# Optimization experiments

Measured on AMD Instinct MI355X. Metric: run time of the kernel, lower is better.

The kernel has to match this reference:

```python
import jax, jax.numpy as jnp
import numpy as np

D_MODEL = 256
B, H, T = 4, 8, 2048
EPS = 1e-8


def _clinear(x_r, x_i, w_r, w_i, b_r, b_i):
    # complex matmul: (x_r + i x_i) @ (w_r + i w_i)^T + (b_r + i b_i)
    y_r = jnp.matmul(x_r, w_r.T) - jnp.matmul(x_i, w_i.T) + b_r
    y_i = jnp.matmul(x_i, w_r.T) + jnp.matmul(x_r, w_i.T) + b_i
    return y_r, y_i


def setup_inputs() -> dict:
    key = jax.random.key(0)
    ks = jax.random.split(key, 24)
    d = D_MODEL
    std = np.sqrt(2.0 / (d + d)) / np.sqrt(2.0)  # glorot-ish * 1/sqrt(2) as in _init_weights
    inp = {}
    inp['q_in_r'] = jax.random.normal(ks[0], (B, H, T, d), jnp.float32)
    inp['q_in_i'] = jax.random.normal(ks[1], (B, H, T, d), jnp.float32)
    inp['kv_in_r'] = jax.random.normal(ks[2], (B, H, T, d), jnp.float32)
    inp['kv_in_i'] = jax.random.normal(ks[3], (B, H, T, d), jnp.float32)
    i = 4
    for p in ['q', 'k', 'v', 'o']:
        inp[p + '_wr'] = std * jax.random.normal(ks[i], (d, d), jnp.float32); i += 1
        inp[p + '_wi'] = std * jax.random.normal(ks[i], (d, d), jnp.float32); i += 1
        inp[p + '_br'] = jnp.zeros((d,), jnp.float32)
        inp[p + '_bi'] = jnp.zeros((d,), jnp.float32)
    inp['gate_w'] = std * jax.random.normal(ks[i], (d, d), jnp.float32)
    inp['gate_b'] = jnp.zeros((d,), jnp.float32)
    return inp


def reference(q_in_r, q_in_i, kv_in_r, kv_in_i,
              q_wr, q_wi, q_br, q_bi,
              k_wr, k_wi, k_br, k_bi,
              v_wr, v_wi, v_br, v_bi,
              o_wr, o_wi, o_br, o_bi,
              gate_w, gate_b):
    D = q_in_r.shape[-1]
    q_r, q_i = _clinear(q_in_r, q_in_i, q_wr, q_wi, q_br, q_bi)
    k_r, k_i = _clinear(kv_in_r, kv_in_i, k_wr, k_wi, k_br, k_bi)
    v_r, v_i = _clinear(kv_in_r, kv_in_i, v_wr, v_wi, v_br, v_bi)
    scale = 1.0 / np.sqrt(D)
    # real part of complex inner product <q, k> (the module's dual-part score)
    scores = (jnp.einsum('bhqd,bhkd->bhqk', q_r, k_r)
              + jnp.einsum('bhqd,bhkd->bhqk', q_i, k_i)) * scale
    attn = jax.nn.softmax(scores, axis=-1)
    ctx_r = jnp.einsum('bhqk,bhkd->bhqd', attn, v_r)
    ctx_i = jnp.einsum('bhqk,bhkd->bhqd', attn, v_i)
    out_r, out_i = _clinear(ctx_r, ctx_i, o_wr, o_wi, o_br, o_bi)
    out_mag = jnp.sqrt(out_r ** 2 + out_i ** 2 + EPS)
    gate = jax.nn.sigmoid(jnp.matmul(out_mag, gate_w.T) + gate_b)
    return out_r * gate, out_i * gate
```

## Files before the change

### kernel.cpp

```cpp
#include <hip/hip_runtime.h>
#include <hip/hip_bf16.h>
#include <hip/hip_fp16.h>
#include <stdint.h>


#define TSEQ   2048
#define NHEADS 32
#define MTOT   65536
#define DDC    512
#define HCHUNK 8

typedef float    f32x4  __attribute__((ext_vector_type(4)));
typedef _Float16 f16x8  __attribute__((ext_vector_type(8)));
typedef uint16_t u16x4  __attribute__((ext_vector_type(4)));
typedef uint16_t u16x8  __attribute__((ext_vector_type(8)));

__device__ __forceinline__ uint16_t f2h(float f) {
  _Float16 h = (_Float16)f;
  return __builtin_bit_cast(uint16_t, h);
}
__device__ __forceinline__ float h2f(uint16_t u) {
  return (float)__builtin_bit_cast(_Float16, u);
}

__device__ __forceinline__ void gld16(const void* g, void* l) {
  __builtin_amdgcn_global_load_lds(
      (const __attribute__((address_space(1))) uint32_t*)g,
      (__attribute__((address_space(3))) uint32_t*)l, 16, 0, 0);
}

enum { EP_F16Z = 0, EP_PROJ = 1, EP_OUT = 2, EP_GATE = 3 };

template <int EP>
__global__ __launch_bounds__(256, 2) void gemm_bt(
    const uint16_t* __restrict__ A, int lda, long zA,
    const uint16_t* __restrict__ B, int ldb, long zB,
    void* __restrict__ C, int ldc, long zC, int K,
    const float* __restrict__ biasR, const float* __restrict__ biasI,
    float scale, float* __restrict__ outR, float* __restrict__ outI) {
  __shared__ uint16_t lA[128 * 32];
  __shared__ uint16_t lB[128 * 32];
  const int tid  = threadIdx.x;
  const int wave = tid >> 6;
  const int lane = tid & 63;
  const int wr   = (wave >> 1) * 64;
  const int wc   = (wave & 1) * 64;
  const long tm  = (long)blockIdx.y * 128;
  const long tn  = (long)blockIdx.x * 128;
  const uint16_t* Ab = A + (long)blockIdx.z * zA;
  const uint16_t* Bb = B + (long)blockIdx.z * zB;

  f32x4 acc[4][4] = {};

  const int  srow  = wave * 16 + (lane >> 2);
  const int  skoff = (lane & 3) * 8;
  uint16_t* lA0 = &lA[(wave * 16) * 32];
  uint16_t* lA1 = &lA[(64 + wave * 16) * 32];
  uint16_t* lB0 = &lB[(wave * 16) * 32];
  uint16_t* lB1 = &lB[(64 + wave * 16) * 32];

  const int fr = lane & 15;
  const int fk = (lane >> 4) * 8;

  const int nK = K >> 5;
  for (int kb = 0; kb < nK; ++kb) {
    const long k0 = (long)kb * 32 + skoff;
    __syncthreads();
    gld16(Ab + (tm + srow) * (long)lda + k0,      lA0);
    gld16(Ab + (tm + 64 + srow) * (long)lda + k0, lA1);
    gld16(Bb + (tn + srow) * (long)ldb + k0,      lB0);
    gld16(Bb + (tn + 64 + srow) * (long)ldb + k0, lB1);
    __syncthreads();

    f16x8 af[4], bf[4];
#pragma unroll
    for (int i = 0; i < 4; ++i)
      af[i] = *(const f16x8*)&lA[(wr + i * 16 + fr) * 32 + fk];
#pragma unroll
    for (int j = 0; j < 4; ++j)
      bf[j] = *(const f16x8*)&lB[(wc + j * 16 + fr) * 32 + fk];
#pragma unroll
    for (int i = 0; i < 4; ++i)
#pragma unroll
      for (int j = 0; j < 4; ++j)
        acc[i][j] = __builtin_amdgcn_mfma_f32_16x16x32_f16(af[i], bf[j], acc[i][j], 0, 0, 0);
  }

  const int quad = lane >> 4;
#pragma unroll
  for (int i = 0; i < 4; ++i) {
    const long row0 = tm + wr + i * 16 + quad * 4;
#pragma unroll
    for (int j = 0; j < 4; ++j) {
      const int col = (int)tn + wc + j * 16 + fr;
#pragma unroll
      for (int r = 0; r < 4; ++r) {
        float v = acc[i][j][r];
        const long rw = row0 + r;
        if constexpr (EP == EP_F16Z) {
          ((uint16_t*)C + (long)blockIdx.z * zC)[rw * (long)ldc + col] = f2h(v * scale);
        } else if constexpr (EP == EP_PROJ) {
          v += (col < 256) ? biasR[col] : biasI[col - 256];
          ((uint16_t*)C)[rw * (long)ldc + col] = f2h(v);
        } else if constexpr (EP == EP_OUT) {
          if (col < 256) outR[rw * 256 + col]       = v + biasR[col];
          else           outI[rw * 256 + col - 256] = v + biasI[col - 256];
        } else {
          const float g = 1.0f / (1.0f + __expf(-(v + biasR[col])));
          const long o = rw * 256 + col;
          outR[o] *= g;
          outI[o] *= g;
        }
      }
    }
  }
}

__global__ void pack_x(const float* __restrict__ xr, const float* __restrict__ xi,
                       uint16_t* __restrict__ out) {
  const long idx = (long)blockIdx.x * 256 + threadIdx.x;
  const long m  = idx >> 7;
  const int  c4 = (int)(idx & 127) << 2;
  const float* src = (c4 < 256) ? (xr + m * 256 + c4) : (xi + m * 256 + (c4 - 256));
  const float4 v = *(const float4*)src;
  u16x4 o = {f2h(v.x), f2h(v.y), f2h(v.z), f2h(v.w)};
  *(u16x4*)(out + m * 512 + c4) = o;
}

__global__ void pack_w(const float* __restrict__ wr, const float* __restrict__ wi,
                       uint16_t* __restrict__ out) {
  const int idx = blockIdx.x * 256 + threadIdx.x;
  const int j  = idx >> 7;
  const int c4 = (idx & 127) << 2;
  const float* src;
  float sgn = 1.f;
  if (j < 256) {
    if (c4 < 256) src = wr + j * 256 + c4;
    else { src = wi + j * 256 + (c4 - 256); sgn = -1.f; }
  } else {
    if (c4 < 256) src = wi + (j - 256) * 256 + c4;
    else          src = wr + (j - 256) * 256 + (c4 - 256);
  }
  const float4 v = *(const float4*)src;
  u16x4 o = {f2h(sgn * v.x), f2h(sgn * v.y), f2h(sgn * v.z), f2h(sgn * v.w)};
  *(u16x4*)(out + (long)j * 512 + c4) = o;
}

__global__ void pack_gw(const float* __restrict__ w, uint16_t* __restrict__ out) {
  const int idx = blockIdx.x * 256 + threadIdx.x;
  const float4 v = *(const float4*)(w + (long)idx * 4);
  u16x4 o = {f2h(v.x), f2h(v.y), f2h(v.z), f2h(v.w)};
  *(u16x4*)(out + (long)idx * 4) = o;
}

__global__ void transpose_v(const uint16_t* __restrict__ V, uint16_t* __restrict__ Vt) {
  __shared__ uint16_t t[32][33];
  const int h = blockIdx.z;
  const uint16_t* Vh = V + (long)h * TSEQ * DDC;
  uint16_t* Vth = Vt + (long)h * DDC * TSEQ;
  const int t0 = blockIdx.x * 32;
  const int n0 = blockIdx.y * 32;
  const int lx = threadIdx.x & 31, ly = threadIdx.x >> 5;
#pragma unroll
  for (int yy = ly; yy < 32; yy += 8)
    t[yy][lx] = Vh[(long)(t0 + yy) * DDC + n0 + lx];
  __syncthreads();
#pragma unroll
  for (int yy = ly; yy < 32; yy += 8)
    Vth[(long)(n0 + yy) * TSEQ + t0 + lx] = t[lx][yy];
}

__global__ __launch_bounds__(256) void softmax_rows(uint16_t* __restrict__ S) {
  const long row = blockIdx.x;
  uint16_t* p = S + row * 2048;
  const int tid = threadIdx.x;
  u16x8 raw = ((const u16x8*)p)[tid];
  float v[8];
#pragma unroll
  for (int j = 0; j < 8; ++j) v[j] = h2f(raw[j]);
  float m = v[0];
#pragma unroll
  for (int j = 1; j < 8; ++j) m = fmaxf(m, v[j]);
#pragma unroll
  for (int off = 32; off >= 1; off >>= 1) m = fmaxf(m, __shfl_xor(m, off));
  __shared__ float red[8];
  const int wave = tid >> 6, lane = tid & 63;
  if (lane == 0) red[wave] = m;
  __syncthreads();
  m = fmaxf(fmaxf(red[0], red[1]), fmaxf(red[2], red[3]));
  float s = 0.f;
#pragma unroll
  for (int j = 0; j < 8; ++j) { v[j] = __expf(v[j] - m); s += v[j]; }
#pragma unroll
  for (int off = 32; off >= 1; off >>= 1) s += __shfl_xor(s, off);
  if (lane == 0) red[4 + wave] = s;
  __syncthreads();
  s = red[4] + red[5] + red[6] + red[7];
  const float inv = 1.0f / s;
  u16x8 o;
#pragma unroll
  for (int j = 0; j < 8; ++j) o[j] = f2h(v[j] * inv);
  ((u16x8*)p)[tid] = o;
}

__global__ void mag_kernel(const float* __restrict__ R, const float* __restrict__ I,
                           uint16_t* __restrict__ mag) {
  const long i = ((long)blockIdx.x * 256 + threadIdx.x) * 4;
  const float4 r  = *(const float4*)(R + i);
  const float4 im = *(const float4*)(I + i);
  u16x4 o = {f2h(sqrtf(r.x * r.x + im.x * im.x + 1e-8f)),
             f2h(sqrtf(r.y * r.y + im.y * im.y + 1e-8f)),
             f2h(sqrtf(r.z * r.z + im.z * im.z + 1e-8f)),
             f2h(sqrtf(r.w * r.w + im.w * im.w + 1e-8f))};
  *(u16x4*)(mag + i) = o;
}

extern "C" void kernel_launch(void* const* d_in, const int* in_sizes, int n_in,
                              void* d_out, int out_size, void* d_ws, size_t ws_size,
                              hipStream_t stream) {
  const float* q_in_r  = (const float*)d_in[0];
  const float* q_in_i  = (const float*)d_in[1];
  const float* kv_in_r = (const float*)d_in[2];
  const float* kv_in_i = (const float*)d_in[3];
  const float* q_wr = (const float*)d_in[4];
  const float* q_wi = (const float*)d_in[5];
  const float* q_br = (const float*)d_in[6];
  const float* q_bi = (const float*)d_in[7];
  const float* k_wr = (const float*)d_in[8];
  const float* k_wi = (const float*)d_in[9];
  const float* k_br = (const float*)d_in[10];
  const float* k_bi = (const float*)d_in[11];
  const float* v_wr = (const float*)d_in[12];
  const float* v_wi = (const float*)d_in[13];
  const float* v_br = (const float*)d_in[14];
  const float* v_bi = (const float*)d_in[15];
  const float* o_wr = (const float*)d_in[16];
  const float* o_wi = (const float*)d_in[17];
  const float* o_br = (const float*)d_in[18];
  const float* o_bi = (const float*)d_in[19];
  const float* gate_w = (const float*)d_in[20];
  const float* gate_b = (const float*)d_in[21];

  unsigned char* w = (unsigned char*)d_ws;
  const size_t MAT16 = (size_t)MTOT * DDC * 2;
  size_t off = 0;
  uint16_t* R1 = (uint16_t*)(w + off); off += MAT16;
  uint16_t* R2 = (uint16_t*)(w + off); off += MAT16;
  uint16_t* R3 = (uint16_t*)(w + off); off += MAT16;
  uint16_t* R4 = (uint16_t*)(w + off); off += MAT16;
  uint16_t* R5 = (uint16_t*)(w + off); off += MAT16;
  uint16_t* Wq = (uint16_t*)(w + off); off += 512 * 512 * 2;
  uint16_t* Wk = (uint16_t*)(w + off); off += 512 * 512 * 2;
  uint16_t* Wv = (uint16_t*)(w + off); off += 512 * 512 * 2;
  uint16_t* Wo = (uint16_t*)(w + off); off += 512 * 512 * 2;
  uint16_t* Gw = (uint16_t*)(w + off); off += 256 * 256 * 2;

  uint16_t* Xq  = R1; uint16_t* Vt  = R1;
  uint16_t* Xkv = R2; uint16_t* Ctx = R2;
  uint16_t* Qm  = R3; uint16_t* Mag = R3;
  uint16_t* Km  = R4;
  uint16_t* Vm  = R5; uint16_t* Sc  = R5;

  float* outR = (float*)d_out;
  float* outI = (float*)d_out + (long)MTOT * 256;

  pack_x<<<32768, 256, 0, stream>>>(q_in_r, q_in_i, Xq);
  pack_x<<<32768, 256, 0, stream>>>(kv_in_r, kv_in_i, Xkv);
  pack_w<<<256, 256, 0, stream>>>(q_wr, q_wi, Wq);
  pack_w<<<256, 256, 0, stream>>>(k_wr, k_wi, Wk);
  pack_w<<<256, 256, 0, stream>>>(v_wr, v_wi, Wv);
  pack_w<<<256, 256, 0, stream>>>(o_wr, o_wi, Wo);
  pack_gw<<<64, 256, 0, stream>>>(gate_w, Gw);

  gemm_bt<EP_PROJ><<<dim3(4, 512, 1), 256, 0, stream>>>(
      Xq, 512, 0, Wq, 512, 0, Qm, 512, 0, 512, q_br, q_bi, 1.f, nullptr, nullptr);
  gemm_bt<EP_PROJ><<<dim3(4, 512, 1), 256, 0, stream>>>(
      Xkv, 512, 0, Wk, 512, 0, Km, 512, 0, 512, k_br, k_bi, 1.f, nullptr, nullptr);
  gemm_bt<EP_PROJ><<<dim3(4, 512, 1), 256, 0, stream>>>(
      Xkv, 512, 0, Wv, 512, 0, Vm, 512, 0, 512, v_br, v_bi, 1.f, nullptr, nullptr);
  transpose_v<<<dim3(64, 16, 32), 256, 0, stream>>>(Vm, Vt);

  for (int c = 0; c < NHEADS / HCHUNK; ++c) {
    const long ho = (long)c * HCHUNK;
    gemm_bt<EP_F16Z><<<dim3(16, 16, HCHUNK), 256, 0, stream>>>(
        Qm + ho * TSEQ * DDC, 512, (long)TSEQ * DDC,
        Km + ho * TSEQ * DDC, 512, (long)TSEQ * DDC,
        Sc, TSEQ, (long)TSEQ * TSEQ, 512, nullptr, nullptr, 0.0625f, nullptr, nullptr);
    softmax_rows<<<HCHUNK * TSEQ, 256, 0, stream>>>(Sc);
    gemm_bt<EP_F16Z><<<dim3(4, 16, HCHUNK), 256, 0, stream>>>(
        Sc, TSEQ, (long)TSEQ * TSEQ,
        Vt + ho * DDC * TSEQ, TSEQ, (long)DDC * TSEQ,
        Ctx + ho * TSEQ * DDC, 512, (long)TSEQ * DDC, 2048,
        nullptr, nullptr, 1.f, nullptr, nullptr);
  }

  gemm_bt<EP_OUT><<<dim3(4, 512, 1), 256, 0, stream>>>(
      Ctx, 512, 0, Wo, 512, 0, nullptr, 0, 0, 512, o_br, o_bi, 1.f, outR, outI);

  mag_kernel<<<16384, 256, 0, stream>>>(outR, outI, Mag);

  gemm_bt<EP_GATE><<<dim3(2, 512, 1), 256, 0, stream>>>(
      Mag, 256, 0, Gw, 256, 0, nullptr, 0, 0, 256, gate_b, nullptr, 1.f, outR, outI);
}
```

Measured before the change: 1.261 ms.

## Double-buffer LDS tiles in GEMM to overlap global loads with MFMA

Splits the K-loop into a prefetch stage and a compute stage over two LDS buffers, so the next tile's global-to-LDS loads are issued before the current tile's MFMAs run. This removes one of the two barriers per iteration and hides load latency behind compute. It doubles LDS use per block, to 32KB, which may limit how many blocks fit per CU.

```diff
diff --git a/kernel.cpp b/kernel.cpp
--- a/kernel.cpp
+++ b/kernel.cpp
@@ -38,8 +38,8 @@
     void* __restrict__ C, int ldc, long zC, int K,
     const float* __restrict__ biasR, const float* __restrict__ biasI,
     float scale, float* __restrict__ outR, float* __restrict__ outI) {
-  __shared__ uint16_t lA[128 * 32];
-  __shared__ uint16_t lB[128 * 32];
+  __shared__ uint16_t lA[2 * 128 * 32];
+  __shared__ uint16_t lB[2 * 128 * 32];
   const int tid  = threadIdx.x;
   const int wave = tid >> 6;
   const int lane = tid & 63;
@@ -52,39 +52,52 @@
 
   f32x4 acc[4][4] = {};
 
-  const int  srow  = wave * 16 + (lane >> 2);
-  const int  skoff = (lane & 3) * 8;
-  uint16_t* lA0 = &lA[(wave * 16) * 32];
-  uint16_t* lA1 = &lA[(64 + wave * 16) * 32];
-  uint16_t* lB0 = &lB[(wave * 16) * 32];
-  uint16_t* lB1 = &lB[(64 + wave * 16) * 32];
+  const int  srow    = wave * 16 + (lane >> 2);
+  const int  skoff   = (lane & 3) * 8;
+  const int  ldsoff0 = (wave * 16) * 32;
+  const int  ldsoff1 = (64 + wave * 16) * 32;
 
   const int fr = lane & 15;
   const int fk = (lane >> 4) * 8;
 
   const int nK = K >> 5;
-  for (int kb = 0; kb < nK; ++kb) {
+
+  auto STAGE = [&](int b, int kb) {
     const long k0 = (long)kb * 32 + skoff;
-    __syncthreads();
-    gld16(Ab + (tm + srow) * (long)lda + k0,      lA0);
-    gld16(Ab + (tm + 64 + srow) * (long)lda + k0, lA1);
-    gld16(Bb + (tn + srow) * (long)ldb + k0,      lB0);
-    gld16(Bb + (tn + 64 + srow) * (long)ldb + k0, lB1);
-    __syncthreads();
-
+    const int  bo = b * (128 * 32);
+    gld16(Ab + (tm + srow) * (long)lda + k0,      lA + bo + ldsoff0);
+    gld16(Ab + (tm + 64 + srow) * (long)lda + k0, lA + bo + ldsoff1);
+    gld16(Bb + (tn + srow) * (long)ldb + k0,      lB + bo + ldsoff0);
+    gld16(Bb + (tn + 64 + srow) * (long)ldb + k0, lB + bo + ldsoff1);
+  };
+
+  auto COMPUTE = [&](int b) {
+    const int bo = b * (128 * 32);
     f16x8 af[4], bf[4];
 #pragma unroll
     for (int i = 0; i < 4; ++i)
-      af[i] = *(const f16x8*)&lA[(wr + i * 16 + fr) * 32 + fk];
+      af[i] = *(const f16x8*)&lA[bo + (wr + i * 16 + fr) * 32 + fk];
 #pragma unroll
     for (int j = 0; j < 4; ++j)
-      bf[j] = *(const f16x8*)&lB[(wc + j * 16 + fr) * 32 + fk];
+      bf[j] = *(const f16x8*)&lB[bo + (wc + j * 16 + fr) * 32 + fk];
 #pragma unroll
     for (int i = 0; i < 4; ++i)
 #pragma unroll
       for (int j = 0; j < 4; ++j)
         acc[i][j] = __builtin_amdgcn_mfma_f32_16x16x32_f16(af[i], bf[j], acc[i][j], 0, 0, 0);
+  };
+
+  STAGE(0, 0);
+  __syncthreads();
+
+  int cur = 0;
+  for (int kb = 0; kb < nK - 1; ++kb) {
+    STAGE(cur ^ 1, kb + 1);
+    COMPUTE(cur);
+    __syncthreads();
+    cur ^= 1;
   }
+  COMPUTE(cur);
 
   const int quad = lane >> 4;
 #pragma unroll
```

After: 1.278 ms. Within noise of the previous version (+1.4%).

## Swizzle workgroup order across XCDs and stage fp16 GEMM epilogue through LDS

Applied to the files above, without the earlier changes.

Remaps each block's linear id so consecutive tiles land on the same XCD, which should improve L2 reuse of A/B panels. For the fp16-output epilogues (projection and scaled-score GEMMs), it writes accumulators into swizzled LDS per wave and then emits 16-byte coalesced global stores instead of scattered 2-byte stores. The swizzle assumes power-of-two grid dimensions and a block count divisible by 8. The LDS staging adds extra syncs and LDS traffic.

```diff
diff --git a/kernel.cpp b/kernel.cpp
--- a/kernel.cpp
+++ b/kernel.cpp
@@ -38,26 +38,39 @@
     void* __restrict__ C, int ldc, long zC, int K,
     const float* __restrict__ biasR, const float* __restrict__ biasI,
     float scale, float* __restrict__ outR, float* __restrict__ outI) {
-  __shared__ uint16_t lA[128 * 32];
-  __shared__ uint16_t lB[128 * 32];
+  __shared__ uint16_t lds[2 * 128 * 32];
+  uint16_t* lA = lds;
+  uint16_t* lB = lds + 128 * 32;
   const int tid  = threadIdx.x;
   const int wave = tid >> 6;
   const int lane = tid & 63;
   const int wr   = (wave >> 1) * 64;
   const int wc   = (wave & 1) * 64;
-  const long tm  = (long)blockIdx.y * 128;
-  const long tn  = (long)blockIdx.x * 128;
-  const uint16_t* Ab = A + (long)blockIdx.z * zA;
-  const uint16_t* Bb = B + (long)blockIdx.z * zB;
+
+  const int gx = gridDim.x, gy = gridDim.y;
+  const int nwg = gx * gy * gridDim.z;
+  const int lin = blockIdx.x + gx * (blockIdx.y + gy * blockIdx.z);
+  const int cpx = nwg >> 3;
+  const int swz = (lin & 7) * cpx + (lin >> 3);
+  const int shx = __popc(gx - 1);
+  const int shy = __popc(gy - 1);
+  const int bx = swz & (gx - 1);
+  const int by = (swz >> shx) & (gy - 1);
+  const int bz = swz >> (shx + shy);
+
+  const long tm  = (long)by * 128;
+  const long tn  = (long)bx * 128;
+  const uint16_t* Ab = A + (long)bz * zA;
+  const uint16_t* Bb = B + (long)bz * zB;
 
   f32x4 acc[4][4] = {};
 
   const int  srow  = wave * 16 + (lane >> 2);
   const int  skoff = (lane & 3) * 8;
-  uint16_t* lA0 = &lA[(wave * 16) * 32];
-  uint16_t* lA1 = &lA[(64 + wave * 16) * 32];
-  uint16_t* lB0 = &lB[(wave * 16) * 32];
-  uint16_t* lB1 = &lB[(64 + wave * 16) * 32];
+  uint16_t* lA0 = lA + (wave * 16) * 32;
+  uint16_t* lA1 = lA + (64 + wave * 16) * 32;
+  uint16_t* lB0 = lB + (wave * 16) * 32;
+  uint16_t* lB1 = lB + (64 + wave * 16) * 32;
 
   const int fr = lane & 15;
   const int fk = (lane >> 4) * 8;
@@ -87,29 +100,73 @@
   }
 
   const int quad = lane >> 4;
-#pragma unroll
-  for (int i = 0; i < 4; ++i) {
-    const long row0 = tm + wr + i * 16 + quad * 4;
-#pragma unroll
-    for (int j = 0; j < 4; ++j) {
-      const int col = (int)tn + wc + j * 16 + fr;
-#pragma unroll
-      for (int r = 0; r < 4; ++r) {
-        float v = acc[i][j][r];
-        const long rw = row0 + r;
-        if constexpr (EP == EP_F16Z) {
-          ((uint16_t*)C + (long)blockIdx.z * zC)[rw * (long)ldc + col] = f2h(v * scale);
-        } else if constexpr (EP == EP_PROJ) {
-          v += (col < 256) ? biasR[col] : biasI[col - 256];
-          ((uint16_t*)C)[rw * (long)ldc + col] = f2h(v);
-        } else if constexpr (EP == EP_OUT) {
-          if (col < 256) outR[rw * 256 + col]       = v + biasR[col];
-          else           outI[rw * 256 + col - 256] = v + biasI[col - 256];
-        } else {
-          const float g = 1.0f / (1.0f + __expf(-(v + biasR[col])));
-          const long o = rw * 256 + col;
-          outR[o] *= g;
-          outI[o] *= g;
+
+  if constexpr (EP == EP_F16Z || EP == EP_PROJ) {
+    __syncthreads();
+    char* wreg = (char*)(lds + wave * 2048);
+    uint16_t* Cp = (uint16_t*)C + ((EP == EP_F16Z) ? (long)bz * zC : 0L);
+#pragma unroll
+    for (int p = 0; p < 2; ++p) {
+#pragma unroll
+      for (int jl = 0; jl < 2; ++jl) {
+        const int j = p * 2 + jl;
+#pragma unroll
+        for (int i = 0; i < 4; ++i) {
+#pragma unroll
+          for (int r = 0; r < 4; ++r) {
+            const int row  = i * 16 + quad * 4 + r;
+            const int colv = jl * 16 + fr;
+            int byte = row * 64 + colv * 2;
+            byte ^= ((row >> 2) & 3) << 5;
+            float v = acc[i][j][r];
+            if constexpr (EP == EP_PROJ) {
+              const int col = (int)tn + wc + p * 32 + colv;
+              v += (col < 256) ? biasR[col] : biasI[col - 256];
+            } else {
+              v *= scale;
+            }
+            *(uint16_t*)(wreg + byte) = f2h(v);
+          }
+        }
+      }
+      asm volatile("s_waitcnt lgkmcnt(0)" ::: "memory");
+      __builtin_amdgcn_sched_barrier(0);
+#pragma unroll
+      for (int t4 = 0; t4 < 4; ++t4) {
+        const int row = t4 * 16 + (lane >> 2);
+        const int c   = lane & 3;
+        int byte = row * 64 + c * 16;
+        byte ^= ((row >> 2) & 3) << 5;
+        const u16x8 val = *(const u16x8*)(wreg + byte);
+        const long grow = tm + wr + row;
+        const int  gcol = (int)tn + wc + p * 32 + c * 8;
+        *(u16x8*)(Cp + grow * (long)ldc + gcol) = val;
+      }
+      if (p == 0) {
+        asm volatile("s_waitcnt lgkmcnt(0)" ::: "memory");
+        __builtin_amdgcn_sched_barrier(0);
+      }
+    }
+  } else {
+#pragma unroll
+    for (int i = 0; i < 4; ++i) {
+      const long row0 = tm + wr + i * 16 + quad * 4;
+#pragma unroll
+      for (int j = 0; j < 4; ++j) {
+        const int col = (int)tn + wc + j * 16 + fr;
+#pragma unroll
+        for (int r = 0; r < 4; ++r) {
+          float v = acc[i][j][r];
+          const long rw = row0 + r;
+          if constexpr (EP == EP_OUT) {
+            if (col < 256) outR[rw * 256 + col]       = v + biasR[col];
+            else           outI[rw * 256 + col - 256] = v + biasI[col - 256];
+          } else {
+            const float g = 1.0f / (1.0f + __expf(-(v + biasR[col])));
+            const long o = rw * 256 + col;
+            outR[o] *= g;
+            outI[o] *= g;
+          }
         }
       }
     }
```

Measured after the change: 1.248 ms. Within noise of the previous version (-1.0%).
